# Kernel tuning notes

Hardware: AMD Instinct MI355X
Metric: run time of the kernel (lower is better)

## Reference

```python
import jax, jax.numpy as jnp
import numpy as np

N_LAYERS = 3
NUM_USERS = 100000
NUM_ITEMS = 50000
N_NODES = NUM_USERS + NUM_ITEMS
N_EDGES = 6000000
EMB = 64


def setup_inputs() -> dict:
    key = jax.random.key(0)
    k1, k2, k3, k4, k5, k6, k7 = jax.random.split(key, 7)
    user_indices = jax.random.randint(k1, (1024,), 0, NUM_USERS)
    item_indices = jax.random.randint(k2, (1024,), 0, NUM_ITEMS)
    adj_src = jax.random.randint(k3, (N_EDGES,), 0, N_NODES)
    adj_dst = jax.random.randint(k4, (N_EDGES,), 0, N_NODES)
    # normalized adjacency values (stand-in for D^-1/2 A D^-1/2 entries)
    adj_vals = jax.random.uniform(k5, (N_EDGES,), dtype=jnp.float32) * 0.05
    user_emb = jax.random.normal(k6, (NUM_USERS, EMB), dtype=jnp.float32) * 0.1
    item_emb = jax.random.normal(k7, (NUM_ITEMS, EMB), dtype=jnp.float32) * 0.1
    return {
        "user_indices": user_indices,
        "item_indices": item_indices,
        "adj_src": adj_src,
        "adj_dst": adj_dst,
        "adj_vals": adj_vals,
        "user_emb": user_emb,
        "item_emb": item_emb,
    }


def reference(user_indices, item_indices, adj_src, adj_dst, adj_vals, user_emb, item_emb):
    # LightGCN.computer(): all_emb = cat(users, items); repeated SpMM; mean over layers
    all_emb = jnp.concatenate([user_emb, item_emb], axis=0)  # [N, d]
    n = all_emb.shape[0]
    cur = all_emb
    acc = all_emb  # running sum over layer embeddings (fused, avoids stacking)
    for _ in range(N_LAYERS):
        # SpMM in COO form: out[dst] += val * cur[src]
        msgs = adj_vals[:, None] * cur[adj_src]  # [E, d]
        cur = jax.ops.segment_sum(msgs, adj_dst, num_segments=n)
        acc = acc + cur
    light_out = acc / jnp.float32(N_LAYERS + 1)  # mean over (n_layers+1) embeddings
    # forward() returns cat(all_users, all_items) == light_out
    return light_out
```

## Files before the change

### kernel.cpp

```cpp
#include <hip/hip_runtime.h>


#define NUM_USERS 100000
#define NUM_ITEMS 50000
#define N_NODES   150000
#define EMB       64
#define N_EDGES   6000000

#define ROWS_PER_B 256
#define NBUCKETS   586
#define NROWS_PAD  (NBUCKETS * ROWS_PER_B)
#define PART_BLOCKS 512
#define CHUNK ((N_EDGES + PART_BLOCKS - 1) / PART_BLOCKS)

constexpr int NODE_F4 = N_NODES * EMB / 4;
constexpr int USER_F4 = NUM_USERS * EMB / 4;

typedef float f4v __attribute__((ext_vector_type(4)));

__device__ __forceinline__ float bf2f(unsigned short u) {
    union { unsigned int i; float f; } x; x.i = ((unsigned int)u) << 16; return x.f;
}
__device__ __forceinline__ unsigned short f2bf(float f) {
    union { float f; unsigned int i; } x; x.f = f;
    unsigned int b = x.i;
    return (unsigned short)((b + 0x7FFFu + ((b >> 16) & 1u)) >> 16);
}


__global__ void k_zero(int* __restrict__ p, int n) {
    int i = blockIdx.x * blockDim.x + threadIdx.x;
    if (i < n) p[i] = 0;
}

__global__ __launch_bounds__(256) void k_bhist(const int* __restrict__ dst,
                                               int* __restrict__ gcnt) {
    __shared__ int cnt[NBUCKETS];
    int t = threadIdx.x;
    for (int i = t; i < NBUCKETS; i += 256) cnt[i] = 0;
    __syncthreads();
    int e0 = blockIdx.x * CHUNK;
    int e1 = min(e0 + CHUNK, N_EDGES);
    int e = e0 + t;
    for (; e + 7 * 256 < e1; e += 8 * 256) {
        int b_[8];
#pragma unroll
        for (int j = 0; j < 8; ++j)
            b_[j] = __builtin_nontemporal_load(dst + e + j * 256) >> 8;
#pragma unroll
        for (int j = 0; j < 8; ++j) atomicAdd(&cnt[b_[j]], 1);
    }
    for (; e < e1; e += 256)
        atomicAdd(&cnt[__builtin_nontemporal_load(dst + e) >> 8], 1);
    __syncthreads();
    for (int i = t; i < NBUCKETS; i += 256)
        if (cnt[i]) atomicAdd(&gcnt[i], cnt[i]);
}

__global__ void k_bscan(const int* __restrict__ gcnt, int* __restrict__ boff,
                        int* __restrict__ gcur) {
    __shared__ int s[1024];
    int t = threadIdx.x;
    int x = (t < NBUCKETS) ? gcnt[t] : 0;
    s[t] = x;
    __syncthreads();
    for (int off = 1; off < 1024; off <<= 1) {
        int v = (t >= off) ? s[t - off] : 0;
        __syncthreads();
        s[t] += v;
        __syncthreads();
    }
    if (t < NBUCKETS) { int ex = s[t] - x; boff[t] = ex; gcur[t] = ex; }
    if (t == 0) boff[NBUCKETS] = N_EDGES;
}


__global__ __launch_bounds__(256) void k_part(const int* __restrict__ src,
                                              const int* __restrict__ dst,
                                              const float* __restrict__ val,
                                              int* __restrict__ gcur,
                                              int2* __restrict__ pairs) {
    __shared__ int cnt[NBUCKETS];
    __shared__ int base[NBUCKETS];
    int t = threadIdx.x;
    for (int i = t; i < NBUCKETS; i += 256) cnt[i] = 0;
    __syncthreads();
    int e0 = blockIdx.x * CHUNK;
    int e1 = min(e0 + CHUNK, N_EDGES);
    {
        int e = e0 + t;
        for (; e + 7 * 256 < e1; e += 8 * 256) {
            int b_[8];
#pragma unroll
            for (int j = 0; j < 8; ++j)
                b_[j] = __builtin_nontemporal_load(dst + e + j * 256) >> 8;
#pragma unroll
            for (int j = 0; j < 8; ++j) atomicAdd(&cnt[b_[j]], 1);
        }
        for (; e < e1; e += 256)
            atomicAdd(&cnt[__builtin_nontemporal_load(dst + e) >> 8], 1);
    }
    __syncthreads();
    for (int i = t; i < NBUCKETS; i += 256) {
        int c = cnt[i];
        base[i] = c ? atomicAdd(&gcur[i], c) : 0;
        cnt[i] = 0;
    }
    __syncthreads();
    {
        int e = e0 + t;
        for (; e + 7 * 256 < e1; e += 8 * 256) {
            int d_[8], s_[8];
            float v_[8];
#pragma unroll
            for (int j = 0; j < 8; ++j)
                d_[j] = __builtin_nontemporal_load(dst + e + j * 256);
#pragma unroll
            for (int j = 0; j < 8; ++j)
                s_[j] = __builtin_nontemporal_load(src + e + j * 256);
#pragma unroll
            for (int j = 0; j < 8; ++j)
                v_[j] = __builtin_nontemporal_load(val + e + j * 256);
#pragma unroll
            for (int j = 0; j < 8; ++j) {
                int b_ = d_[j] >> 8;
                int o = atomicAdd(&cnt[b_], 1);
                pairs[base[b_] + o] = make_int2(s_[j] | ((d_[j] & 255) << 18),
                                                __float_as_int(v_[j]));
            }
        }
        for (; e < e1; e += 256) {
            int d0 = __builtin_nontemporal_load(dst + e);
            int s0 = __builtin_nontemporal_load(src + e);
            float v0 = __builtin_nontemporal_load(val + e);
            int b_ = d0 >> 8;
            int o0 = atomicAdd(&cnt[b_], 1);
            pairs[base[b_] + o0] = make_int2(s0 | ((d0 & 255) << 18),
                                             __float_as_int(v0));
        }
    }
}


__global__ __launch_bounds__(512) void k_sort(const int* __restrict__ boff,
                                              const int2* __restrict__ pairs1,
                                              int2* __restrict__ pairs2,
                                              int* __restrict__ row_ptr) {
    __shared__ int cnt[ROWS_PER_B];
    __shared__ int s[ROWS_PER_B];
    int b = blockIdx.x;
    int t = threadIdx.x;
    if (t < ROWS_PER_B) cnt[t] = 0;
    __syncthreads();
    int beg = boff[b], end = boff[b + 1];
    {
        int e = beg + t;
        for (; e + 7 * 512 < end; e += 8 * 512) {
            int r_[8];
#pragma unroll
            for (int j = 0; j < 8; ++j)
                r_[j] = ((unsigned)pairs1[e + j * 512].x) >> 18;
#pragma unroll
            for (int j = 0; j < 8; ++j) atomicAdd(&cnt[r_[j]], 1);
        }
        for (; e < end; e += 512)
            atomicAdd(&cnt[((unsigned)pairs1[e].x) >> 18], 1);
    }
    __syncthreads();
    int x = (t < ROWS_PER_B) ? cnt[t] : 0;
    if (t < ROWS_PER_B) s[t] = x;
    __syncthreads();
    for (int off = 1; off < ROWS_PER_B; off <<= 1) {
        int v = (t >= off && t < ROWS_PER_B) ? s[t - off] : 0;
        __syncthreads();
        if (t < ROWS_PER_B) s[t] += v;
        __syncthreads();
    }
    if (t < ROWS_PER_B) {
        int ex = beg + s[t] - x;
        row_ptr[b * ROWS_PER_B + t] = ex;
        cnt[t] = ex;
    }
    if (b == NBUCKETS - 1 && t == ROWS_PER_B - 1) row_ptr[NROWS_PAD] = N_EDGES;
    __syncthreads();
    const long* p1l = (const long*)pairs1;
    {
        int e = beg + t;
        for (; e + 7 * 512 < end; e += 8 * 512) {
            long q[8];
#pragma unroll
            for (int j = 0; j < 8; ++j)
                q[j] = __builtin_nontemporal_load(p1l + e + j * 512);
#pragma unroll
            for (int j = 0; j < 8; ++j) {
                int x0 = (int)q[j], y0 = (int)(q[j] >> 32);
                int pos = atomicAdd(&cnt[((unsigned)x0) >> 18], 1);
                pairs2[pos] = make_int2(x0 & 0x3FFFF, y0);
            }
        }
        for (; e < end; e += 512) {
            long q0 = __builtin_nontemporal_load(p1l + e);
            int x0 = (int)q0, y0 = (int)(q0 >> 32);
            int pos = atomicAdd(&cnt[((unsigned)x0) >> 18], 1);
            pairs2[pos] = make_int2(x0 & 0x3FFFF, y0);
        }
    }
}


__global__ void k_init(const f4v* __restrict__ ue, const f4v* __restrict__ ie,
                       ushort4* __restrict__ e0b, f4v* __restrict__ acc) {
    int i = blockIdx.x * blockDim.x + threadIdx.x;
    if (i >= NODE_F4) return;
    f4v v = (i < USER_F4) ? __builtin_nontemporal_load(ue + i)
                          : __builtin_nontemporal_load(ie + i - USER_F4);
    __builtin_nontemporal_store(v, acc + i);
    e0b[i] = make_ushort4(f2bf(v.x), f2bf(v.y), f2bf(v.z), f2bf(v.w));
}

__global__ __launch_bounds__(256) void k_spmm(const int* __restrict__ row_ptr,
                                              const long* __restrict__ pairs,
                                              const ushort4* __restrict__ cur,
                                              ushort4* __restrict__ nxt) {
    int tid = blockIdx.x * blockDim.x + threadIdx.x;
    int row = tid >> 4;
    if (row >= N_NODES) return;
    int c = tid & 15;
    int beg = row_ptr[row];
    int end = row_ptr[row + 1];
    float4 r = make_float4(0.f, 0.f, 0.f, 0.f);
    int k = beg;
    for (; k + 7 < end; k += 8) {
        long p[8];
        ushort4 g[8];
#pragma unroll
        for (int j = 0; j < 8; ++j) p[j] = pairs[k + j];
#pragma unroll
        for (int j = 0; j < 8; ++j) g[j] = cur[(long)(int)(p[j] & 0x3FFFF) * 16 + c];
#pragma unroll
        for (int j = 0; j < 8; ++j) {
            float v = __int_as_float((int)(p[j] >> 32));
            r.x += v * bf2f(g[j].x);
            r.y += v * bf2f(g[j].y);
            r.z += v * bf2f(g[j].z);
            r.w += v * bf2f(g[j].w);
        }
    }
    for (; k < end; ++k) {
        long p0 = pairs[k];
        ushort4 g0 = cur[(long)(int)(p0 & 0x3FFFF) * 16 + c];
        float v0 = __int_as_float((int)(p0 >> 32));
        r.x += v0 * bf2f(g0.x);
        r.y += v0 * bf2f(g0.y);
        r.z += v0 * bf2f(g0.z);
        r.w += v0 * bf2f(g0.w);
    }
    nxt[(long)row * 16 + c] = make_ushort4(f2bf(r.x), f2bf(r.y), f2bf(r.z), f2bf(r.w));
}

__global__ __launch_bounds__(256) void k_spmm_fin(const int* __restrict__ row_ptr,
                                                  const long* __restrict__ pairs,
                                                  const ushort4* __restrict__ cur,
                                                  const ushort4* __restrict__ e1b,
                                                  float4* __restrict__ acc) {
    int tid = blockIdx.x * blockDim.x + threadIdx.x;
    int row = tid >> 4;
    if (row >= N_NODES) return;
    int c = tid & 15;
    int beg = row_ptr[row];
    int end = row_ptr[row + 1];
    float4 r = make_float4(0.f, 0.f, 0.f, 0.f);
    int k = beg;
    for (; k + 7 < end; k += 8) {
        long p[8];
        ushort4 g[8];
#pragma unroll
        for (int j = 0; j < 8; ++j) p[j] = pairs[k + j];
#pragma unroll
        for (int j = 0; j < 8; ++j) g[j] = cur[(long)(int)(p[j] & 0x3FFFF) * 16 + c];
#pragma unroll
        for (int j = 0; j < 8; ++j) {
            float v = __int_as_float((int)(p[j] >> 32));
            r.x += v * bf2f(g[j].x);
            r.y += v * bf2f(g[j].y);
            r.z += v * bf2f(g[j].z);
            r.w += v * bf2f(g[j].w);
        }
    }
    for (; k < end; ++k) {
        long p0 = pairs[k];
        ushort4 g0 = cur[(long)(int)(p0 & 0x3FFFF) * 16 + c];
        float v0 = __int_as_float((int)(p0 >> 32));
        r.x += v0 * bf2f(g0.x);
        r.y += v0 * bf2f(g0.y);
        r.z += v0 * bf2f(g0.z);
        r.w += v0 * bf2f(g0.w);
    }
    long o = (long)row * 16 + c;
    ushort4 e1 = e1b[o];
    ushort4 e2 = cur[o];
    float4 a = acc[o];
    a.x = (a.x + bf2f(e1.x) + bf2f(e2.x) + r.x) * 0.25f;
    a.y = (a.y + bf2f(e1.y) + bf2f(e2.y) + r.y) * 0.25f;
    a.z = (a.z + bf2f(e1.z) + bf2f(e2.z) + r.z) * 0.25f;
    a.w = (a.w + bf2f(e1.w) + bf2f(e2.w) + r.w) * 0.25f;
    acc[o] = a;
}


__global__ void lgcn_init(const float4* __restrict__ user_emb,
                          const float4* __restrict__ item_emb,
                          float4* __restrict__ cur, float4* __restrict__ nxt,
                          float4* __restrict__ acc) {
    int i = blockIdx.x * blockDim.x + threadIdx.x;
    if (i >= NODE_F4) return;
    float4 v = (i < USER_F4) ? user_emb[i] : item_emb[i - USER_F4];
    cur[i] = v; acc[i] = v; nxt[i] = make_float4(0.f, 0.f, 0.f, 0.f);
}

__global__ void lgcn_scatter(const int* __restrict__ src, const int* __restrict__ dst,
                             const float* __restrict__ val,
                             const float4* __restrict__ cur, float* __restrict__ nxt) {
    int tid = blockIdx.x * blockDim.x + threadIdx.x;
    int e = tid >> 4;
    if (e >= N_EDGES) return;
    int c = tid & 15;
    int s = src[e]; int d = dst[e]; float v = val[e];
    float4 m = cur[(long)s * 16 + c];
    float* p = nxt + (long)d * 64 + c * 4;
    unsafeAtomicAdd(p + 0, v * m.x);
    unsafeAtomicAdd(p + 1, v * m.y);
    unsafeAtomicAdd(p + 2, v * m.z);
    unsafeAtomicAdd(p + 3, v * m.w);
}

__global__ void lgcn_add_zero(float4* __restrict__ acc, const float4* __restrict__ nxt,
                              float4* __restrict__ other) {
    int i = blockIdx.x * blockDim.x + threadIdx.x;
    if (i >= NODE_F4) return;
    float4 a = acc[i]; float4 n = nxt[i];
    a.x += n.x; a.y += n.y; a.z += n.z; a.w += n.w;
    acc[i] = a;
    other[i] = make_float4(0.f, 0.f, 0.f, 0.f);
}

__global__ void lgcn_final(float4* __restrict__ acc, const float4* __restrict__ nxt) {
    int i = blockIdx.x * blockDim.x + threadIdx.x;
    if (i >= NODE_F4) return;
    float4 a = acc[i]; float4 n = nxt[i];
    a.x = (a.x + n.x) * 0.25f; a.y = (a.y + n.y) * 0.25f;
    a.z = (a.z + n.z) * 0.25f; a.w = (a.w + n.w) * 0.25f;
    acc[i] = a;
}


extern "C" void kernel_launch(void* const* d_in, const int* in_sizes, int n_in,
                              void* d_out, int out_size, void* d_ws, size_t ws_size,
                              hipStream_t stream) {
    const int*    adj_src  = (const int*)d_in[2];
    const int*    adj_dst  = (const int*)d_in[3];
    const float*  adj_vals = (const float*)d_in[4];
    float* acc = (float*)d_out;

    const int BLK = 256;
    const int grid_node  = (NODE_F4 + BLK - 1) / BLK;
    const int grid_row16 = (N_NODES * 16 + BLK - 1) / BLK;

    const size_t SZ_PAIRS = (size_t)N_EDGES * 8;
    const size_t SZ_BF    = (size_t)N_NODES * EMB * 2;
    const size_t SZ_RP    = 600320;
    const size_t SZ_B     = 4096;
    const size_t NEEDED   = 2 * SZ_PAIRS + SZ_BF + SZ_RP + 3 * SZ_B;

    if (ws_size >= NEEDED) {
        char* w = (char*)d_ws;
        int2*    pairs2 = (int2*)(w);
        int2*    pairs1 = (int2*)(w + SZ_PAIRS);
        ushort4* e0b    = (ushort4*)(w + SZ_PAIRS);
        ushort4* e1b    = (ushort4*)(w + SZ_PAIRS + SZ_BF);
        ushort4* e2b    = (ushort4*)(w + 2 * SZ_PAIRS);
        int*  row_ptr= (int*)(w + 2 * SZ_PAIRS + SZ_BF);
        int*  gcnt   = (int*)(w + 2 * SZ_PAIRS + SZ_BF + SZ_RP);
        int*  boff   = (int*)(w + 2 * SZ_PAIRS + SZ_BF + SZ_RP + SZ_B);
        int*  gcur   = (int*)(w + 2 * SZ_PAIRS + SZ_BF + SZ_RP + 2 * SZ_B);

        k_zero<<<(NBUCKETS + BLK - 1) / BLK, BLK, 0, stream>>>(gcnt, NBUCKETS);
        k_bhist<<<PART_BLOCKS, BLK, 0, stream>>>(adj_dst, gcnt);
        k_bscan<<<1, 1024, 0, stream>>>(gcnt, boff, gcur);

        k_part<<<PART_BLOCKS, BLK, 0, stream>>>(adj_src, adj_dst, adj_vals, gcur, pairs1);

        k_sort<<<NBUCKETS, 512, 0, stream>>>(boff, pairs1, pairs2, row_ptr);

        k_init<<<grid_node, BLK, 0, stream>>>((const f4v*)d_in[5], (const f4v*)d_in[6],
                                              e0b, (f4v*)acc);
        k_spmm<<<grid_row16, BLK, 0, stream>>>(row_ptr, (const long*)pairs2, e0b, e1b);
        k_spmm<<<grid_row16, BLK, 0, stream>>>(row_ptr, (const long*)pairs2, e1b, e2b);
        k_spmm_fin<<<grid_row16, BLK, 0, stream>>>(row_ptr, (const long*)pairs2, e2b,
                                                   e1b, (float4*)acc);
    } else {
        const float4* user_emb = (const float4*)d_in[5];
        const float4* item_emb = (const float4*)d_in[6];
        float* ws0 = (float*)d_ws;
        float* ws1 = ws0 + (size_t)N_NODES * EMB;
        lgcn_init<<<grid_node, BLK, 0, stream>>>(user_emb, item_emb,
                                                 (float4*)ws0, (float4*)ws1, (float4*)acc);
        lgcn_scatter<<<(N_EDGES*16+BLK-1)/BLK, BLK, 0, stream>>>(adj_src, adj_dst, adj_vals,
                                                    (const float4*)ws0, ws1);
        lgcn_add_zero<<<grid_node, BLK, 0, stream>>>((float4*)acc, (const float4*)ws1, (float4*)ws0);
        lgcn_scatter<<<(N_EDGES*16+BLK-1)/BLK, BLK, 0, stream>>>(adj_src, adj_dst, adj_vals,
                                                    (const float4*)ws1, ws0);
        lgcn_add_zero<<<grid_node, BLK, 0, stream>>>((float4*)acc, (const float4*)ws0, (float4*)ws1);
        lgcn_scatter<<<(N_EDGES*16+BLK-1)/BLK, BLK, 0, stream>>>(adj_src, adj_dst, adj_vals,
                                                    (const float4*)ws0, ws1);
        lgcn_final<<<grid_node, BLK, 0, stream>>>((float4*)acc, (const float4*)ws1);
    }
}
```

Baseline: 628.0 us.

## Replace bucket histogram with global per-row histogram and precomputed row pointers

```diff
diff --git a/kernel.cpp b/kernel.cpp
--- a/kernel.cpp
+++ b/kernel.cpp
@@ -33,28 +33,34 @@
     if (i < n) p[i] = 0;
 }
 
-__global__ __launch_bounds__(256) void k_bhist(const int* __restrict__ dst,
-                                               int* __restrict__ gcnt) {
-    __shared__ int cnt[NBUCKETS];
-    int t = threadIdx.x;
-    for (int i = t; i < NBUCKETS; i += 256) cnt[i] = 0;
-    __syncthreads();
+__global__ __launch_bounds__(256) void k_rhist(const int* __restrict__ dst,
+                                               int* __restrict__ rcnt) {
     int e0 = blockIdx.x * CHUNK;
     int e1 = min(e0 + CHUNK, N_EDGES);
-    int e = e0 + t;
+    int e = e0 + threadIdx.x;
     for (; e + 7 * 256 < e1; e += 8 * 256) {
-        int b_[8];
+        int d_[8];
 #pragma unroll
         for (int j = 0; j < 8; ++j)
-            b_[j] = __builtin_nontemporal_load(dst + e + j * 256) >> 8;
-#pragma unroll
-        for (int j = 0; j < 8; ++j) atomicAdd(&cnt[b_[j]], 1);
+            d_[j] = __builtin_nontemporal_load(dst + e + j * 256);
+#pragma unroll
+        for (int j = 0; j < 8; ++j) atomicAdd(&rcnt[d_[j]], 1);
     }
     for (; e < e1; e += 256)
-        atomicAdd(&cnt[__builtin_nontemporal_load(dst + e) >> 8], 1);
-    __syncthreads();
-    for (int i = t; i < NBUCKETS; i += 256)
-        if (cnt[i]) atomicAdd(&gcnt[i], cnt[i]);
+        atomicAdd(&rcnt[__builtin_nontemporal_load(dst + e)], 1);
+}
+
+__global__ __launch_bounds__(256) void k_bsum(const int* __restrict__ rcnt,
+                                              int* __restrict__ gcnt) {
+    __shared__ int s[256];
+    int b = blockIdx.x, t = threadIdx.x;
+    s[t] = rcnt[b * 256 + t];
+    __syncthreads();
+    for (int off = 128; off > 0; off >>= 1) {
+        if (t < off) s[t] += s[t + off];
+        __syncthreads();
+    }
+    if (t == 0) gcnt[b] = s[0];
 }
 
 __global__ void k_bscan(const int* __restrict__ gcnt, int* __restrict__ boff,
@@ -72,6 +78,24 @@
     }
     if (t < NBUCKETS) { int ex = s[t] - x; boff[t] = ex; gcur[t] = ex; }
     if (t == 0) boff[NBUCKETS] = N_EDGES;
+}
+
+__global__ __launch_bounds__(256) void k_rscan(const int* __restrict__ rcnt,
+                                               const int* __restrict__ boff,
+                                               int* __restrict__ row_ptr) {
+    __shared__ int s[256];
+    int b = blockIdx.x, t = threadIdx.x;
+    int x = rcnt[b * 256 + t];
+    s[t] = x;
+    __syncthreads();
+    for (int off = 1; off < 256; off <<= 1) {
+        int v = (t >= off) ? s[t - off] : 0;
+        __syncthreads();
+        s[t] += v;
+        __syncthreads();
+    }
+    row_ptr[b * 256 + t] = boff[b] + s[t] - x;
+    if (b == NBUCKETS - 1 && t == 255) row_ptr[NROWS_PAD] = N_EDGES;
 }
 
 
@@ -143,67 +167,34 @@
 
 
 __global__ __launch_bounds__(512) void k_sort(const int* __restrict__ boff,
+                                              const int* __restrict__ row_ptr,
                                               const int2* __restrict__ pairs1,
-                                              int2* __restrict__ pairs2,
-                                              int* __restrict__ row_ptr) {
+                                              int2* __restrict__ pairs2) {
     __shared__ int cnt[ROWS_PER_B];
-    __shared__ int s[ROWS_PER_B];
     int b = blockIdx.x;
     int t = threadIdx.x;
-    if (t < ROWS_PER_B) cnt[t] = 0;
+    if (t < ROWS_PER_B) cnt[t] = row_ptr[b * ROWS_PER_B + t];
     __syncthreads();
     int beg = boff[b], end = boff[b + 1];
-    {
-        int e = beg + t;
-        for (; e + 7 * 512 < end; e += 8 * 512) {
-            int r_[8];
-#pragma unroll
-            for (int j = 0; j < 8; ++j)
-                r_[j] = ((unsigned)pairs1[e + j * 512].x) >> 18;
-#pragma unroll
-            for (int j = 0; j < 8; ++j) atomicAdd(&cnt[r_[j]], 1);
-        }
-        for (; e < end; e += 512)
-            atomicAdd(&cnt[((unsigned)pairs1[e].x) >> 18], 1);
-    }
-    __syncthreads();
-    int x = (t < ROWS_PER_B) ? cnt[t] : 0;
-    if (t < ROWS_PER_B) s[t] = x;
-    __syncthreads();
-    for (int off = 1; off < ROWS_PER_B; off <<= 1) {
-        int v = (t >= off && t < ROWS_PER_B) ? s[t - off] : 0;
-        __syncthreads();
-        if (t < ROWS_PER_B) s[t] += v;
-        __syncthreads();
-    }
-    if (t < ROWS_PER_B) {
-        int ex = beg + s[t] - x;
-        row_ptr[b * ROWS_PER_B + t] = ex;
-        cnt[t] = ex;
-    }
-    if (b == NBUCKETS - 1 && t == ROWS_PER_B - 1) row_ptr[NROWS_PAD] = N_EDGES;
-    __syncthreads();
     const long* p1l = (const long*)pairs1;
-    {
-        int e = beg + t;
-        for (; e + 7 * 512 < end; e += 8 * 512) {
-            long q[8];
-#pragma unroll
-            for (int j = 0; j < 8; ++j)
-                q[j] = __builtin_nontemporal_load(p1l + e + j * 512);
-#pragma unroll
-            for (int j = 0; j < 8; ++j) {
-                int x0 = (int)q[j], y0 = (int)(q[j] >> 32);
-                int pos = atomicAdd(&cnt[((unsigned)x0) >> 18], 1);
-                pairs2[pos] = make_int2(x0 & 0x3FFFF, y0);
-            }
-        }
-        for (; e < end; e += 512) {
-            long q0 = __builtin_nontemporal_load(p1l + e);
-            int x0 = (int)q0, y0 = (int)(q0 >> 32);
+    int e = beg + t;
+    for (; e + 7 * 512 < end; e += 8 * 512) {
+        long q[8];
+#pragma unroll
+        for (int j = 0; j < 8; ++j)
+            q[j] = __builtin_nontemporal_load(p1l + e + j * 512);
+#pragma unroll
+        for (int j = 0; j < 8; ++j) {
+            int x0 = (int)q[j], y0 = (int)(q[j] >> 32);
             int pos = atomicAdd(&cnt[((unsigned)x0) >> 18], 1);
             pairs2[pos] = make_int2(x0 & 0x3FFFF, y0);
         }
+    }
+    for (; e < end; e += 512) {
+        long q0 = __builtin_nontemporal_load(p1l + e);
+        int x0 = (int)q0, y0 = (int)(q0 >> 32);
+        int pos = atomicAdd(&cnt[((unsigned)x0) >> 18], 1);
+        pairs2[pos] = make_int2(x0 & 0x3FFFF, y0);
     }
 }
 
@@ -375,6 +366,7 @@
     if (ws_size >= NEEDED) {
         char* w = (char*)d_ws;
         int2*    pairs2 = (int2*)(w);
+        int*     rcnt   = (int*)(w);
         int2*    pairs1 = (int2*)(w + SZ_PAIRS);
         ushort4* e0b    = (ushort4*)(w + SZ_PAIRS);
         ushort4* e1b    = (ushort4*)(w + SZ_PAIRS + SZ_BF);
@@ -384,13 +376,15 @@
         int*  boff   = (int*)(w + 2 * SZ_PAIRS + SZ_BF + SZ_RP + SZ_B);
         int*  gcur   = (int*)(w + 2 * SZ_PAIRS + SZ_BF + SZ_RP + 2 * SZ_B);
 
-        k_zero<<<(NBUCKETS + BLK - 1) / BLK, BLK, 0, stream>>>(gcnt, NBUCKETS);
-        k_bhist<<<PART_BLOCKS, BLK, 0, stream>>>(adj_dst, gcnt);
+        k_zero<<<(NROWS_PAD + BLK - 1) / BLK, BLK, 0, stream>>>(rcnt, NROWS_PAD);
+        k_rhist<<<PART_BLOCKS, BLK, 0, stream>>>(adj_dst, rcnt);
+        k_bsum<<<NBUCKETS, BLK, 0, stream>>>(rcnt, gcnt);
         k_bscan<<<1, 1024, 0, stream>>>(gcnt, boff, gcur);
+        k_rscan<<<NBUCKETS, BLK, 0, stream>>>(rcnt, boff, row_ptr);
 
         k_part<<<PART_BLOCKS, BLK, 0, stream>>>(adj_src, adj_dst, adj_vals, gcur, pairs1);
 
-        k_sort<<<NBUCKETS, 512, 0, stream>>>(boff, pairs1, pairs2, row_ptr);
+        k_sort<<<NBUCKETS, 512, 0, stream>>>(boff, row_ptr, pairs1, pairs2);
 
         k_init<<<grid_node, BLK, 0, stream>>>((const f4v*)d_in[5], (const f4v*)d_in[6],
                                               e0b, (f4v*)acc);
```

Result: slower. 840.0 us (+33.8%).

## Drop bucket histogram pass with fixed-capacity buckets and fuse initial embedding into final

Applied to the files above, without the earlier changes.

```diff
diff --git a/kernel.cpp b/kernel.cpp
--- a/kernel.cpp
+++ b/kernel.cpp
@@ -7,11 +7,12 @@
 #define EMB       64
 #define N_EDGES   6000000
 
-#define ROWS_PER_B 256
-#define NBUCKETS   586
-#define NROWS_PAD  (NBUCKETS * ROWS_PER_B)
+#define RPB       293
+#define NBUCKETS  512
+#define NROWS_PAD (NBUCKETS * RPB)
 #define PART_BLOCKS 512
 #define CHUNK ((N_EDGES + PART_BLOCKS - 1) / PART_BLOCKS)
+#define CAP_B 12480
 
 constexpr int NODE_F4 = N_NODES * EMB / 4;
 constexpr int USER_F4 = NUM_USERS * EMB / 4;
@@ -28,52 +29,10 @@
 }
 
 
-__global__ void k_zero(int* __restrict__ p, int n) {
-    int i = blockIdx.x * blockDim.x + threadIdx.x;
-    if (i < n) p[i] = 0;
-}
-
-__global__ __launch_bounds__(256) void k_bhist(const int* __restrict__ dst,
-                                               int* __restrict__ gcnt) {
-    __shared__ int cnt[NBUCKETS];
-    int t = threadIdx.x;
-    for (int i = t; i < NBUCKETS; i += 256) cnt[i] = 0;
-    __syncthreads();
-    int e0 = blockIdx.x * CHUNK;
-    int e1 = min(e0 + CHUNK, N_EDGES);
-    int e = e0 + t;
-    for (; e + 7 * 256 < e1; e += 8 * 256) {
-        int b_[8];
-#pragma unroll
-        for (int j = 0; j < 8; ++j)
-            b_[j] = __builtin_nontemporal_load(dst + e + j * 256) >> 8;
-#pragma unroll
-        for (int j = 0; j < 8; ++j) atomicAdd(&cnt[b_[j]], 1);
-    }
-    for (; e < e1; e += 256)
-        atomicAdd(&cnt[__builtin_nontemporal_load(dst + e) >> 8], 1);
-    __syncthreads();
-    for (int i = t; i < NBUCKETS; i += 256)
-        if (cnt[i]) atomicAdd(&gcnt[i], cnt[i]);
-}
-
-__global__ void k_bscan(const int* __restrict__ gcnt, int* __restrict__ boff,
-                        int* __restrict__ gcur) {
-    __shared__ int s[1024];
-    int t = threadIdx.x;
-    int x = (t < NBUCKETS) ? gcnt[t] : 0;
-    s[t] = x;
-    __syncthreads();
-    for (int off = 1; off < 1024; off <<= 1) {
-        int v = (t >= off) ? s[t - off] : 0;
-        __syncthreads();
-        s[t] += v;
-        __syncthreads();
-    }
-    if (t < NBUCKETS) { int ex = s[t] - x; boff[t] = ex; gcur[t] = ex; }
-    if (t == 0) boff[NBUCKETS] = N_EDGES;
-}
-
+__global__ void k_ginit(int* __restrict__ gcur) {
+    int i = blockIdx.x * blockDim.x + threadIdx.x;
+    if (i < NBUCKETS) gcur[i] = i * CAP_B;
+}
 
 __global__ __launch_bounds__(256) void k_part(const int* __restrict__ src,
                                               const int* __restrict__ dst,
@@ -93,12 +52,12 @@
             int b_[8];
 #pragma unroll
             for (int j = 0; j < 8; ++j)
-                b_[j] = __builtin_nontemporal_load(dst + e + j * 256) >> 8;
+                b_[j] = (int)((unsigned)__builtin_nontemporal_load(dst + e + j * 256) / (unsigned)RPB);
 #pragma unroll
             for (int j = 0; j < 8; ++j) atomicAdd(&cnt[b_[j]], 1);
         }
         for (; e < e1; e += 256)
-            atomicAdd(&cnt[__builtin_nontemporal_load(dst + e) >> 8], 1);
+            atomicAdd(&cnt[(unsigned)__builtin_nontemporal_load(dst + e) / (unsigned)RPB], 1);
     }
     __syncthreads();
     for (int i = t; i < NBUCKETS; i += 256) {
@@ -123,9 +82,10 @@
                 v_[j] = __builtin_nontemporal_load(val + e + j * 256);
 #pragma unroll
             for (int j = 0; j < 8; ++j) {
-                int b_ = d_[j] >> 8;
+                int b_ = (int)((unsigned)d_[j] / (unsigned)RPB);
+                int lo = d_[j] - b_ * RPB;
                 int o = atomicAdd(&cnt[b_], 1);
-                pairs[base[b_] + o] = make_int2(s_[j] | ((d_[j] & 255) << 18),
+                pairs[base[b_] + o] = make_int2(s_[j] | (lo << 18),
                                                 __float_as_int(v_[j]));
             }
         }
@@ -133,64 +93,82 @@
             int d0 = __builtin_nontemporal_load(dst + e);
             int s0 = __builtin_nontemporal_load(src + e);
             float v0 = __builtin_nontemporal_load(val + e);
-            int b_ = d0 >> 8;
+            int b_ = (int)((unsigned)d0 / (unsigned)RPB);
+            int lo = d0 - b_ * RPB;
             int o0 = atomicAdd(&cnt[b_], 1);
-            pairs[base[b_] + o0] = make_int2(s0 | ((d0 & 255) << 18),
+            pairs[base[b_] + o0] = make_int2(s0 | (lo << 18),
                                              __float_as_int(v0));
         }
     }
 }
 
-
-__global__ __launch_bounds__(512) void k_sort(const int* __restrict__ boff,
-                                              const int2* __restrict__ pairs1,
-                                              int2* __restrict__ pairs2,
-                                              int* __restrict__ row_ptr) {
-    __shared__ int cnt[ROWS_PER_B];
-    __shared__ int s[ROWS_PER_B];
+__global__ void k_fill(const int* __restrict__ gcur, int* __restrict__ boff) {
+    __shared__ int s[1024];
+    int t = threadIdx.x;
+    int x = (t < NBUCKETS) ? (gcur[t] - t * CAP_B) : 0;
+    s[t] = x;
+    __syncthreads();
+    for (int off = 1; off < 1024; off <<= 1) {
+        int v = (t >= off) ? s[t - off] : 0;
+        __syncthreads();
+        s[t] += v;
+        __syncthreads();
+    }
+    if (t < NBUCKETS) boff[t] = s[t] - x;
+    if (t == 0) boff[NBUCKETS] = N_EDGES;
+}
+
+__global__ __launch_bounds__(1024) void k_sortA(const int* __restrict__ gcur,
+                                                const int* __restrict__ boff,
+                                                const int2* __restrict__ pairs1,
+                                                int2* __restrict__ pairs2,
+                                                int* __restrict__ row_ptr) {
+    __shared__ int cnt[RPB];
+    __shared__ int s[RPB];
     int b = blockIdx.x;
     int t = threadIdx.x;
-    if (t < ROWS_PER_B) cnt[t] = 0;
-    __syncthreads();
-    int beg = boff[b], end = boff[b + 1];
+    if (t < RPB) cnt[t] = 0;
+    __syncthreads();
+    int beg = b * CAP_B;
+    int end = gcur[b];
     {
         int e = beg + t;
-        for (; e + 7 * 512 < end; e += 8 * 512) {
+        for (; e + 7 * 1024 < end; e += 8 * 1024) {
             int r_[8];
 #pragma unroll
             for (int j = 0; j < 8; ++j)
-                r_[j] = ((unsigned)pairs1[e + j * 512].x) >> 18;
+                r_[j] = ((unsigned)pairs1[e + j * 1024].x) >> 18;
 #pragma unroll
             for (int j = 0; j < 8; ++j) atomicAdd(&cnt[r_[j]], 1);
         }
-        for (; e < end; e += 512)
+        for (; e < end; e += 1024)
             atomicAdd(&cnt[((unsigned)pairs1[e].x) >> 18], 1);
     }
     __syncthreads();
-    int x = (t < ROWS_PER_B) ? cnt[t] : 0;
-    if (t < ROWS_PER_B) s[t] = x;
-    __syncthreads();
-    for (int off = 1; off < ROWS_PER_B; off <<= 1) {
-        int v = (t >= off && t < ROWS_PER_B) ? s[t - off] : 0;
+    int x = (t < RPB) ? cnt[t] : 0;
+    if (t < RPB) s[t] = x;
+    __syncthreads();
+    for (int off = 1; off < RPB; off <<= 1) {
+        int v = (t >= off && t < RPB) ? s[t - off] : 0;
         __syncthreads();
-        if (t < ROWS_PER_B) s[t] += v;
+        if (t < RPB) s[t] += v;
         __syncthreads();
     }
-    if (t < ROWS_PER_B) {
-        int ex = beg + s[t] - x;
-        row_ptr[b * ROWS_PER_B + t] = ex;
+    if (t < RPB) {
+        int ex = boff[b] + s[t] - x;
+        row_ptr[b * RPB + t] = ex;
         cnt[t] = ex;
     }
-    if (b == NBUCKETS - 1 && t == ROWS_PER_B - 1) row_ptr[NROWS_PAD] = N_EDGES;
+    if (b == NBUCKETS - 1 && t == 0) row_ptr[NROWS_PAD] = N_EDGES;
     __syncthreads();
     const long* p1l = (const long*)pairs1;
     {
         int e = beg + t;
-        for (; e + 7 * 512 < end; e += 8 * 512) {
+        for (; e + 7 * 1024 < end; e += 8 * 1024) {
             long q[8];
 #pragma unroll
             for (int j = 0; j < 8; ++j)
-                q[j] = __builtin_nontemporal_load(p1l + e + j * 512);
+                q[j] = __builtin_nontemporal_load(p1l + e + j * 1024);
 #pragma unroll
             for (int j = 0; j < 8; ++j) {
                 int x0 = (int)q[j], y0 = (int)(q[j] >> 32);
@@ -198,7 +176,7 @@
                 pairs2[pos] = make_int2(x0 & 0x3FFFF, y0);
             }
         }
-        for (; e < end; e += 512) {
+        for (; e < end; e += 1024) {
             long q0 = __builtin_nontemporal_load(p1l + e);
             int x0 = (int)q0, y0 = (int)(q0 >> 32);
             int pos = atomicAdd(&cnt[((unsigned)x0) >> 18], 1);
@@ -209,12 +187,11 @@
 
 
 __global__ void k_init(const f4v* __restrict__ ue, const f4v* __restrict__ ie,
-                       ushort4* __restrict__ e0b, f4v* __restrict__ acc) {
+                       ushort4* __restrict__ e0b) {
     int i = blockIdx.x * blockDim.x + threadIdx.x;
     if (i >= NODE_F4) return;
     f4v v = (i < USER_F4) ? __builtin_nontemporal_load(ue + i)
                           : __builtin_nontemporal_load(ie + i - USER_F4);
-    __builtin_nontemporal_store(v, acc + i);
     e0b[i] = make_ushort4(f2bf(v.x), f2bf(v.y), f2bf(v.z), f2bf(v.w));
 }
 
@@ -262,6 +239,8 @@
                                                   const long* __restrict__ pairs,
                                                   const ushort4* __restrict__ cur,
                                                   const ushort4* __restrict__ e1b,
+                                                  const f4v* __restrict__ ue,
+                                                  const f4v* __restrict__ ie,
                                                   float4* __restrict__ acc) {
     int tid = blockIdx.x * blockDim.x + threadIdx.x;
     int row = tid >> 4;
@@ -297,13 +276,14 @@
         r.w += v0 * bf2f(g0.w);
     }
     long o = (long)row * 16 + c;
+    f4v e0 = (row < NUM_USERS) ? ue[o] : ie[o - (long)NUM_USERS * 16];
     ushort4 e1 = e1b[o];
     ushort4 e2 = cur[o];
-    float4 a = acc[o];
-    a.x = (a.x + bf2f(e1.x) + bf2f(e2.x) + r.x) * 0.25f;
-    a.y = (a.y + bf2f(e1.y) + bf2f(e2.y) + r.y) * 0.25f;
-    a.z = (a.z + bf2f(e1.z) + bf2f(e2.z) + r.z) * 0.25f;
-    a.w = (a.w + bf2f(e1.w) + bf2f(e2.w) + r.w) * 0.25f;
+    float4 a;
+    a.x = (e0.x + bf2f(e1.x) + bf2f(e2.x) + r.x) * 0.25f;
+    a.y = (e0.y + bf2f(e1.y) + bf2f(e2.y) + r.y) * 0.25f;
+    a.z = (e0.z + bf2f(e1.z) + bf2f(e2.z) + r.z) * 0.25f;
+    a.w = (e0.w + bf2f(e1.w) + bf2f(e2.w) + r.w) * 0.25f;
     acc[o] = a;
 }
 
@@ -367,37 +347,36 @@
     const int grid_row16 = (N_NODES * 16 + BLK - 1) / BLK;
 
     const size_t SZ_PAIRS = (size_t)N_EDGES * 8;
+    const size_t SZ_P1PAD = (size_t)NBUCKETS * CAP_B * 8;
     const size_t SZ_BF    = (size_t)N_NODES * EMB * 2;
     const size_t SZ_RP    = 600320;
     const size_t SZ_B     = 4096;
-    const size_t NEEDED   = 2 * SZ_PAIRS + SZ_BF + SZ_RP + 3 * SZ_B;
-
-    if (ws_size >= NEEDED) {
+    const size_t NEEDED1  = SZ_PAIRS + SZ_P1PAD + SZ_BF + SZ_RP + 2 * SZ_B;
+
+    if (ws_size >= NEEDED1) {
         char* w = (char*)d_ws;
         int2*    pairs2 = (int2*)(w);
         int2*    pairs1 = (int2*)(w + SZ_PAIRS);
         ushort4* e0b    = (ushort4*)(w + SZ_PAIRS);
         ushort4* e1b    = (ushort4*)(w + SZ_PAIRS + SZ_BF);
-        ushort4* e2b    = (ushort4*)(w + 2 * SZ_PAIRS);
-        int*  row_ptr= (int*)(w + 2 * SZ_PAIRS + SZ_BF);
-        int*  gcnt   = (int*)(w + 2 * SZ_PAIRS + SZ_BF + SZ_RP);
-        int*  boff   = (int*)(w + 2 * SZ_PAIRS + SZ_BF + SZ_RP + SZ_B);
-        int*  gcur   = (int*)(w + 2 * SZ_PAIRS + SZ_BF + SZ_RP + 2 * SZ_B);
-
-        k_zero<<<(NBUCKETS + BLK - 1) / BLK, BLK, 0, stream>>>(gcnt, NBUCKETS);
-        k_bhist<<<PART_BLOCKS, BLK, 0, stream>>>(adj_dst, gcnt);
-        k_bscan<<<1, 1024, 0, stream>>>(gcnt, boff, gcur);
-
-        k_part<<<PART_BLOCKS, BLK, 0, stream>>>(adj_src, adj_dst, adj_vals, gcur, pairs1);
-
-        k_sort<<<NBUCKETS, 512, 0, stream>>>(boff, pairs1, pairs2, row_ptr);
+        ushort4* e2b    = (ushort4*)(w + SZ_PAIRS + SZ_P1PAD);
+        int*  row_ptr= (int*)(w + SZ_PAIRS + SZ_P1PAD + SZ_BF);
+        int*  gcur   = (int*)(w + SZ_PAIRS + SZ_P1PAD + SZ_BF + SZ_RP);
+        int*  boff   = (int*)(w + SZ_PAIRS + SZ_P1PAD + SZ_BF + SZ_RP + SZ_B);
+
+        k_ginit<<<(NBUCKETS + BLK - 1) / BLK, BLK, 0, stream>>>(gcur);
+        k_part<<<PART_BLOCKS, BLK, 0, stream>>>(adj_src, adj_dst, adj_vals,
+                                                gcur, pairs1);
+        k_fill<<<1, 1024, 0, stream>>>(gcur, boff);
+        k_sortA<<<NBUCKETS, 1024, 0, stream>>>(gcur, boff, pairs1, pairs2, row_ptr);
 
         k_init<<<grid_node, BLK, 0, stream>>>((const f4v*)d_in[5], (const f4v*)d_in[6],
-                                              e0b, (f4v*)acc);
+                                              e0b);
         k_spmm<<<grid_row16, BLK, 0, stream>>>(row_ptr, (const long*)pairs2, e0b, e1b);
         k_spmm<<<grid_row16, BLK, 0, stream>>>(row_ptr, (const long*)pairs2, e1b, e2b);
         k_spmm_fin<<<grid_row16, BLK, 0, stream>>>(row_ptr, (const long*)pairs2, e2b,
-                                                   e1b, (float4*)acc);
+                                                   e1b, (const f4v*)d_in[5],
+                                                   (const f4v*)d_in[6], (float4*)acc);
     } else {
         const float4* user_emb = (const float4*)d_in[5];
         const float4* item_emb = (const float4*)d_in[6];
```

New measurement: 592.9 us. 5.6% less time.
